# Kernel tuning notes

Measured on AMD Instinct MI355X. Metric: run time of the kernel, lower is better.

The kernel has to match this reference:

```python
import jax, jax.numpy as jnp
import numpy as np

EMB = 16      # importance embedding channels (ch 0 = logit, 1: = cov features)
NSEG = 196    # n_segments (14x14 superpixel grid)
MC = 16       # num_monte_carlo
TEMP = 1.0    # initial Gumbel/RelaxedBernoulli temperature (compute_temperature(0))
JITTER = 1e-3 # numerical_stability_check: diagonal jitter so Cholesky succeeds


def setup_inputs() -> dict:
    key = jax.random.key(0)
    k1, k2, k3 = jax.random.split(key, 3)
    B, C, H, W = 16, 3, 224, 224
    x = jax.random.normal(k1, (B, C, H, W), jnp.float32)
    groups = jax.random.randint(k2, (B, H, W), 0, NSEG, jnp.int32)
    W_conv = jax.random.normal(k3, (EMB, C), jnp.float32) * 0.1
    b_conv = jnp.zeros((EMB,), jnp.float32)
    return {"x": x, "groups": groups, "W_conv": W_conv, "b_conv": b_conv}


def _group_mean(groups, emb):
    # scatter_reduce(mean, include_self=False): per-batch segment mean, 0 for empty groups
    # emb: [B,E,H,W], groups: [B,H,W] -> [B, NSEG, E]
    B, E, H, W = emb.shape
    flat = emb.reshape(B, E, H * W).transpose(0, 2, 1).reshape(B * H * W, E)
    ids = (groups.reshape(B, H * W).astype(jnp.int32)
           + NSEG * jnp.arange(B, dtype=jnp.int32)[:, None]).reshape(-1)
    sums = jax.ops.segment_sum(flat, ids, num_segments=B * NSEG).reshape(B, NSEG, E)
    cnt = jax.ops.segment_sum(jnp.ones((B * H * W,), flat.dtype), ids,
                              num_segments=B * NSEG).reshape(B, NSEG, 1)
    return sums / jnp.maximum(cnt, 1.0)


def reference(x, groups, W_conv, b_conv):
    B, C, H, W = x.shape
    # importance_predictor as 1x1 conv: [B,C,H,W] -> [B,EMB,H,W]
    emb = jnp.einsum('bchw,ec->behw', x, W_conv) + b_conv[None, :, None, None]

    avg = _group_mean(groups, emb)            # [B, NSEG, EMB]
    mu = avg[:, :, 0]                          # [B, NSEG]
    gemb = avg[:, :, 1:]                       # [B, NSEG, EMB-1]
    # groups_emb.mT @ groups_emb (groups_emb is [B, EMB-1, NSEG] in torch)
    sigma = jnp.einsum('bse,bte->bst', gemb, gemb)
    sigma = sigma + JITTER * jnp.eye(NSEG, dtype=sigma.dtype)

    pixel_probs = jax.nn.sigmoid(emb[:, 0])    # [B, H, W]
    group_probs = jax.nn.sigmoid(mu)           # [B, NSEG]

    # MultivariateNormal(mu, sigma).rsample([MC]).movedim(0,-1)
    L = jnp.linalg.cholesky(sigma)             # [B, NSEG, NSEG]
    kg, ku = jax.random.split(jax.random.key(42))
    eps = jax.random.normal(kg, (B, NSEG, MC), x.dtype)
    logits_mc = mu[:, :, None] + jnp.einsum('bst,btm->bsm', L, eps)  # [B,NSEG,MC]

    # RelaxedBernoulli(temp, probs=sigmoid(logits_mc)).rsample()
    u = jax.random.uniform(ku, (B, NSEG, MC), x.dtype, 1e-6, 1.0 - 1e-6)
    logistic = jnp.log(u) - jnp.log1p(-u)
    relaxed = jax.nn.sigmoid((logits_mc + logistic) / TEMP)
    hard = (relaxed > 0.5).astype(relaxed.dtype)
    groups_mcmc = hard + relaxed - jax.lax.stop_gradient(relaxed)  # straight-through

    # groups_to_mask: gather group decision back to every pixel
    gf = groups.reshape(B, H * W).astype(jnp.int32)
    idx = jnp.broadcast_to(gf[:, :, None], (B, H * W, MC))
    mask = jnp.take_along_axis(groups_mcmc, idx, axis=1)           # [B, HW, MC]
    mask = mask.reshape(B, H, W, MC)
    mask = jnp.broadcast_to(mask[:, None], (B, C, H, W, MC))       # expand channels
    return mask, group_probs, pixel_probs, sigma
```

## Files before the change

kernel.cpp:

```cpp
#include <hip/hip_runtime.h>
#include <stdint.h>

#define HW    50176
#define BATCH 16
#define NSEG  196
#define EMB   16
#define MC    16
#define JITTER 0.001f
#define EBLK  14
#define PXB   3584

__host__ __device__ inline void threefry2x32(uint32_t k0, uint32_t k1,
                                             uint32_t x0, uint32_t x1,
                                             uint32_t& o0, uint32_t& o1) {
  uint32_t k2 = k0 ^ k1 ^ 0x1BD11BDAu;
#define TFR(r) { x0 += x1; x1 = (x1 << (r)) | (x1 >> (32 - (r))); x1 ^= x0; }
  x0 += k0; x1 += k1;
  TFR(13) TFR(15) TFR(26) TFR(6)
  x0 += k1; x1 += k2 + 1u;
  TFR(17) TFR(29) TFR(16) TFR(24)
  x0 += k2; x1 += k0 + 2u;
  TFR(13) TFR(15) TFR(26) TFR(6)
  x0 += k0; x1 += k1 + 3u;
  TFR(17) TFR(29) TFR(16) TFR(24)
  x0 += k1; x1 += k2 + 4u;
  TFR(13) TFR(15) TFR(26) TFR(6)
  x0 += k2; x1 += k0 + 5u;
#undef TFR
  o0 = x0; o1 = x1;
}

__device__ inline float erfinv_f32(float x) {
  float w = -log1pf(-x * x);
  float p;
  if (w < 5.0f) {
    w = w - 2.5f;
    p = 2.81022636e-08f;
    p = 3.43273939e-07f + p * w;
    p = -3.5233877e-06f + p * w;
    p = -4.39150654e-06f + p * w;
    p = 0.00021858087f + p * w;
    p = -0.00125372503f + p * w;
    p = -0.00417768164f + p * w;
    p = 0.246640727f + p * w;
    p = 1.50140941f + p * w;
  } else {
    w = sqrtf(w) - 3.0f;
    p = -0.000200214257f;
    p = 0.000100950558f + p * w;
    p = 0.00134934322f + p * w;
    p = -0.00367342844f + p * w;
    p = 0.00573950773f + p * w;
    p = -0.0076224613f + p * w;
    p = 0.00943887047f + p * w;
    p = 1.00167406f + p * w;
    p = 2.83297682f + p * w;
  }
  return p * x;
}

__device__ inline float bits_to_f01(uint32_t bits) {
  uint32_t fb = (bits >> 9) | 0x3F800000u;
  return __uint_as_float(fb) - 1.0f;
}

__device__ inline float dot15(const float a[15], const float b[15]) {
  float d = 0.0f;
#pragma unroll
  for (int j = 0; j < 15; ++j) d = fmaf(a[j], b[j], d);
  return d;
}

__device__ inline void pivot_scalars(const float gk[15], float& invd,
                                     float& dd, float& beta) {
  const float sj = 0.031622776601683794f;
  float t0 = fmaf(gk[0], gk[0], JITTER);
  float t1 = gk[1] * gk[1];   float t2 = gk[2] * gk[2];
  float t3 = gk[3] * gk[3];   float t4 = gk[4] * gk[4];
  float t5 = gk[5] * gk[5];   float t6 = gk[6] * gk[6];
  float t7 = gk[7] * gk[7];   float t8 = gk[8] * gk[8];
  float t9 = gk[9] * gk[9];   float t10 = gk[10] * gk[10];
  float t11 = gk[11] * gk[11]; float t12 = gk[12] * gk[12];
  float t13 = gk[13] * gk[13]; float t14 = gk[14] * gk[14];
  float u0 = t0 + t1, u1 = t2 + t3, u2 = t4 + t5, u3 = t6 + t7;
  float u4 = t8 + t9, u5 = t10 + t11, u6 = t12 + t13;
  float v0 = u0 + u1, v1 = u2 + u3, v2 = u4 + u5, v3 = u6 + t14;
  float jn = (v0 + v1) + (v2 + v3);
  invd = __builtin_amdgcn_rsqf(jn);
  dd = jn * invd;
  beta = (invd * invd) * __builtin_amdgcn_rcpf(fmaf(sj, invd, 1.0f));
}

__global__ __launch_bounds__(256) void emb_kernel(
    const float* __restrict__ x, const int* __restrict__ groups,
    const float* __restrict__ Wc, const float* __restrict__ bc,
    float* __restrict__ partial, float* __restrict__ pixel_probs) {
  __shared__ float lsum[4 * NSEG];
  int b = blockIdx.x / EBLK;
  int blk = blockIdx.x % EBLK;
  int tid = threadIdx.x;
  for (int i = tid; i < 4 * NSEG; i += 256) lsum[i] = 0.0f;
  __syncthreads();
  const float* xb = x + (size_t)b * 3 * HW;
  float w0 = Wc[0], w1 = Wc[1], w2 = Wc[2], b0 = bc[0];
  for (int k = 0; k < PXB / 256; ++k) {
    int p = blk * PXB + k * 256 + tid;
    float x0 = xb[p], x1 = xb[HW + p], x2 = xb[2 * HW + p];
    int g = groups[b * HW + p];
    float e = w0 * x0 + w1 * x1;
    e = e + w2 * x2 + b0;
    pixel_probs[b * HW + p] = 1.0f / (1.0f + expf(-e));
    atomicAdd(&lsum[g], x0);
    atomicAdd(&lsum[NSEG + g], x1);
    atomicAdd(&lsum[2 * NSEG + g], x2);
    atomicAdd(&lsum[3 * NSEG + g], 1.0f);
  }
  __syncthreads();
  float* pb = partial + (size_t)blockIdx.x * (4 * NSEG);
  if (tid < NSEG) {
#pragma unroll
    for (int c = 0; c < 4; ++c) pb[c * NSEG + tid] = lsum[c * NSEG + tid];
  }
}

__global__ __launch_bounds__(256, 1) void main_kernel(
    const float* __restrict__ partial, const float* __restrict__ Wc,
    const float* __restrict__ bc,
    uint32_t kg0, uint32_t kg1, uint32_t ku0, uint32_t ku1,
    float* __restrict__ group_probs, float* __restrict__ sigma_out,
    float* __restrict__ hard) {
  int bid = blockIdx.x;
  int tid = threadIdx.x;

  if (bid < 112) {
    int b = bid / 7;
    int tile = bid % 7;
    __shared__ float ge_s[15][NSEG];
    if (tid < NSEG) {
      float sx0 = 0.0f, sx1 = 0.0f, sx2 = 0.0f, cn = 0.0f;
      for (int bb = 0; bb < EBLK; ++bb) {
        const float* pb = partial + (size_t)(b * EBLK + bb) * (4 * NSEG);
        sx0 += pb[tid]; sx1 += pb[NSEG + tid];
        sx2 += pb[2 * NSEG + tid]; cn += pb[3 * NSEG + tid];
      }
      float denom = fmaxf(cn, 1.0f);
#pragma unroll
      for (int j = 1; j < EMB; ++j) {
        float e = Wc[j * 3 + 0] * sx0 + Wc[j * 3 + 1] * sx1;
        e = e + Wc[j * 3 + 2] * sx2 + bc[j] * cn;
        ge_s[j - 1][tid] = e / denom;
      }
    }
    __syncthreads();
    if (tid < NSEG) {
      int t = tid;
      float gt[15];
#pragma unroll
      for (int j = 0; j < 15; ++j) gt[j] = ge_s[j][t];
      for (int r = 0; r < 28; ++r) {
        int s = tile * 28 + r;
        float a = 0.0f;
#pragma unroll
        for (int j = 0; j < 15; ++j) a = fmaf(ge_s[j][s], gt[j], a);
        if (s == t) a += JITTER;
        sigma_out[((size_t)b * NSEG + s) * NSEG + t] = a;
      }
    }
    return;
  }

  int b = bid - 112;
  __shared__ float ge[15][NSEG];
  __shared__ float mu_l[NSEG];
  __shared__ float eps_lds[NSEG * MC];
  __shared__ __align__(16) float pbuf[2][4][16];

  for (int t = tid; t < NSEG * MC; t += 256) {
    uint32_t a0, a1;
    threefry2x32(kg0, kg1, 0u, (uint32_t)(b * NSEG * MC + t), a0, a1);
    float f = bits_to_f01(a0 ^ a1);
    const float lo = -0.99999994f;
    float u = fmaxf(lo, f * (1.0f - lo) + lo);
    eps_lds[t] = 1.4142135623730951f * erfinv_f32(u);
  }

  if (tid < NSEG) {
    float sx0 = 0.0f, sx1 = 0.0f, sx2 = 0.0f, cn = 0.0f;
    for (int bb = 0; bb < EBLK; ++bb) {
      const float* pb = partial + (size_t)(b * EBLK + bb) * (4 * NSEG);
      sx0 += pb[tid]; sx1 += pb[NSEG + tid];
      sx2 += pb[2 * NSEG + tid]; cn += pb[3 * NSEG + tid];
    }
    float denom = fmaxf(cn, 1.0f);
#pragma unroll
    for (int j = 0; j < EMB; ++j) {
      float e = Wc[j * 3 + 0] * sx0 + Wc[j * 3 + 1] * sx1;
      e = e + Wc[j * 3 + 2] * sx2 + bc[j] * cn;
      float v = e / denom;
      if (j == 0) {
        mu_l[tid] = v;
        group_probs[b * NSEG + tid] = 1.0f / (1.0f + expf(-v));
      } else {
        ge[j - 1][tid] = v;
      }
    }
  }
  __syncthreads();

  int i = tid;
  float g[15];
#pragma unroll
  for (int j = 0; j < 15; ++j) g[j] = (i < NSEG) ? ge[j][i] : 0.0f;
  float acc[16];
#pragma unroll
  for (int m = 0; m < 16; ++m) acc[m] = 0.0f;
  if (tid < 4) {
    float* pw = &pbuf[0][tid][0];
#pragma unroll
    for (int j = 0; j < 15; ++j) pw[j] = g[j];
  }
  __syncthreads();

#define APPLY_PIVOT(rv, invd_, dd_, beta_, K)                               \
  {                                                                         \
    float dot = dot15(g, rv);                                               \
    float w = (i > (K)) ? dot * (invd_)                                     \
                        : ((i == (K)) ? (dd_) : 0.0f);                      \
    const float4* ep = (const float4*)(eps_lds + (K) * MC);                 \
    float4 e0 = ep[0], e1 = ep[1], e2 = ep[2], e3 = ep[3];                  \
    float ek[16] = {e0.x, e0.y, e0.z, e0.w, e1.x, e1.y, e1.z, e1.w,         \
                    e2.x, e2.y, e2.z, e2.w, e3.x, e3.y, e3.z, e3.w};        \
    _Pragma("unroll")                                                       \
    for (int m = 0; m < 16; ++m) acc[m] = fmaf(w, ek[m], acc[m]);           \
    float bd = (beta_) * dot;                                               \
    _Pragma("unroll")                                                       \
    for (int j = 0; j < 15; ++j) g[j] = fmaf(-bd, rv[j], g[j]);             \
  }

  for (int t49 = 0; t49 < 49; ++t49) {
    const float* pb0 = &pbuf[t49 & 1][0][0];
    float r0[15], r1[15], r2[15], r3[15];
    {
      float4 a0 = *(const float4*)(pb0 + 0);
      float4 a1 = *(const float4*)(pb0 + 4);
      float4 a2 = *(const float4*)(pb0 + 8);
      float4 a3 = *(const float4*)(pb0 + 12);
      r0[0]=a0.x; r0[1]=a0.y; r0[2]=a0.z; r0[3]=a0.w;
      r0[4]=a1.x; r0[5]=a1.y; r0[6]=a1.z; r0[7]=a1.w;
      r0[8]=a2.x; r0[9]=a2.y; r0[10]=a2.z; r0[11]=a2.w;
      r0[12]=a3.x; r0[13]=a3.y; r0[14]=a3.z;
      a0 = *(const float4*)(pb0 + 16); a1 = *(const float4*)(pb0 + 20);
      a2 = *(const float4*)(pb0 + 24); a3 = *(const float4*)(pb0 + 28);
      r1[0]=a0.x; r1[1]=a0.y; r1[2]=a0.z; r1[3]=a0.w;
      r1[4]=a1.x; r1[5]=a1.y; r1[6]=a1.z; r1[7]=a1.w;
      r1[8]=a2.x; r1[9]=a2.y; r1[10]=a2.z; r1[11]=a2.w;
      r1[12]=a3.x; r1[13]=a3.y; r1[14]=a3.z;
      a0 = *(const float4*)(pb0 + 32); a1 = *(const float4*)(pb0 + 36);
      a2 = *(const float4*)(pb0 + 40); a3 = *(const float4*)(pb0 + 44);
      r2[0]=a0.x; r2[1]=a0.y; r2[2]=a0.z; r2[3]=a0.w;
      r2[4]=a1.x; r2[5]=a1.y; r2[6]=a1.z; r2[7]=a1.w;
      r2[8]=a2.x; r2[9]=a2.y; r2[10]=a2.z; r2[11]=a2.w;
      r2[12]=a3.x; r2[13]=a3.y; r2[14]=a3.z;
      a0 = *(const float4*)(pb0 + 48); a1 = *(const float4*)(pb0 + 52);
      a2 = *(const float4*)(pb0 + 56); a3 = *(const float4*)(pb0 + 60);
      r3[0]=a0.x; r3[1]=a0.y; r3[2]=a0.z; r3[3]=a0.w;
      r3[4]=a1.x; r3[5]=a1.y; r3[6]=a1.z; r3[7]=a1.w;
      r3[8]=a2.x; r3[9]=a2.y; r3[10]=a2.z; r3[11]=a2.w;
      r3[12]=a3.x; r3[13]=a3.y; r3[14]=a3.z;
    }
    float invd0, dd0, beta0, invd1, dd1, beta1;
    float invd2, dd2, beta2, invd3, dd3, beta3;
    pivot_scalars(r0, invd0, dd0, beta0);
    {
      float d = dot15(r1, r0); float bd = beta0 * d;
#pragma unroll
      for (int j = 0; j < 15; ++j) r1[j] = fmaf(-bd, r0[j], r1[j]);
    }
    pivot_scalars(r1, invd1, dd1, beta1);
    {
      float d = dot15(r2, r0); float bd = beta0 * d;
#pragma unroll
      for (int j = 0; j < 15; ++j) r2[j] = fmaf(-bd, r0[j], r2[j]);
      d = dot15(r2, r1); bd = beta1 * d;
#pragma unroll
      for (int j = 0; j < 15; ++j) r2[j] = fmaf(-bd, r1[j], r2[j]);
    }
    pivot_scalars(r2, invd2, dd2, beta2);
    {
      float d = dot15(r3, r0); float bd = beta0 * d;
#pragma unroll
      for (int j = 0; j < 15; ++j) r3[j] = fmaf(-bd, r0[j], r3[j]);
      d = dot15(r3, r1); bd = beta1 * d;
#pragma unroll
      for (int j = 0; j < 15; ++j) r3[j] = fmaf(-bd, r1[j], r3[j]);
      d = dot15(r3, r2); bd = beta2 * d;
#pragma unroll
      for (int j = 0; j < 15; ++j) r3[j] = fmaf(-bd, r2[j], r3[j]);
    }
    pivot_scalars(r3, invd3, dd3, beta3);

    int k0 = 4 * t49;
    APPLY_PIVOT(r0, invd0, dd0, beta0, k0 + 0)
    APPLY_PIVOT(r1, invd1, dd1, beta1, k0 + 1)
    APPLY_PIVOT(r2, invd2, dd2, beta2, k0 + 2)
    APPLY_PIVOT(r3, invd3, dd3, beta3, k0 + 3)

    int nb = 4 * (t49 + 1);
    if (i >= nb && i < nb + 4) {
      float* pw = &pbuf[(t49 + 1) & 1][i - nb][0];
#pragma unroll
      for (int j = 0; j < 15; ++j) pw[j] = g[j];
    }
    __syncthreads();
  }
#undef APPLY_PIVOT

  if (i < NSEG) {
    float mui = mu_l[i];
    float4 outv[4];
    float* op = (float*)outv;
#pragma unroll
    for (int m = 0; m < 16; ++m) {
      uint32_t a0, a1;
      threefry2x32(ku0, ku1, 0u, (uint32_t)(b * NSEG * MC + i * MC + m), a0, a1);
      float f = bits_to_f01(a0 ^ a1);
      const float mn = 1e-6f;
      const float mx = (float)(1.0 - 1e-6);
      float uu = fmaxf(mn, f * (mx - mn) + mn);
      float lg = logf(uu) - log1pf(-uu);
      float z = mui + acc[m] + lg;
      op[m] = (z > 0.0f) ? 1.0f : 0.0f;
    }
    float4* hp = (float4*)(hard + ((size_t)b * NSEG + i) * MC);
#pragma unroll
    for (int q = 0; q < 4; ++q) hp[q] = outv[q];
  }
}

__global__ __launch_bounds__(256) void mask_kernel(
    const int* __restrict__ groups, const float* __restrict__ hard,
    float4* __restrict__ out) {
  int f = blockIdx.x * blockDim.x + threadIdx.x;
  if (f >= BATCH * 3 * HW * 4) return;
  int pix = f >> 2;
  int q = f & 3;
  int b = pix / (3 * HW);
  int p = pix % HW;
  int g = groups[b * HW + p];
  out[f] = ((const float4*)hard)[(b * NSEG + g) * 4 + q];
}

extern "C" void kernel_launch(void* const* d_in, const int* in_sizes, int n_in,
                              void* d_out, int out_size, void* d_ws, size_t ws_size,
                              hipStream_t stream) {
  const float* x = (const float*)d_in[0];
  const int* groups = (const int*)d_in[1];
  const float* Wc = (const float*)d_in[2];
  const float* bc = (const float*)d_in[3];

  float* out = (float*)d_out;
  float* mask_out = out;
  float* gp_out = out + 38535168;
  float* pp_out = gp_out + 3136;
  float* sig_out = pp_out + 802816;

  float* ws = (float*)d_ws;
  float* partial = ws;
  float* hard    = ws + 175616;

  emb_kernel<<<BATCH * EBLK, 256, 0, stream>>>(x, groups, Wc, bc, partial, pp_out);

  uint32_t kg0, kg1, ku0, ku1;
  threefry2x32(0u, 42u, 0u, 0u, kg0, kg1);
  threefry2x32(0u, 42u, 0u, 1u, ku0, ku1);

  main_kernel<<<128, 256, 0, stream>>>(partial, Wc, bc, kg0, kg1, ku0, ku1,
                                       gp_out, sig_out, hard);
  mask_kernel<<<(BATCH * 3 * HW * 4 + 255) / 256, 256, 0, stream>>>(
      groups, hard, (float4*)mask_out);
}
```

Baseline: 252.2 us.

## Factor next Cholesky panel in owning wave via readlane lookahead

Replaces the per-step redundant 4-row panel factorization done by every thread with a lookahead scheme. The wave that owns the next four pivot rows factors them using readlane broadcasts and publishes the pivot rows and scalars to LDS. All other waves then just apply the published panel. This removes redundant per-thread pivot computation and overlaps panel factorization with the trailing update. In exchange the owning wave does extra serial work and the barrier count is unchanged.

Measured after the change: 262.1 us. 3.9% more time.

```diff
diff --git a/kernel.cpp b/kernel.cpp
--- a/kernel.cpp
+++ b/kernel.cpp
@@ -64,6 +64,10 @@
   return __uint_as_float(fb) - 1.0f;
 }
 
+__device__ inline float readlane_f(float v, int lane) {
+  return __int_as_float(__builtin_amdgcn_readlane(__float_as_int(v), lane));
+}
+
 __device__ inline float dot15(const float a[15], const float b[15]) {
   float d = 0.0f;
 #pragma unroll
@@ -170,10 +174,12 @@
   }
 
   int b = bid - 112;
+  int lane = tid & 63;
+  int wave = tid >> 6;
   __shared__ float ge[15][NSEG];
   __shared__ float mu_l[NSEG];
   __shared__ float eps_lds[NSEG * MC];
-  __shared__ __align__(16) float pbuf[2][4][16];
+  __shared__ __align__(16) float pfin[2][4][20];
 
   for (int t = tid; t < NSEG * MC; t += 256) {
     uint32_t a0, a1;
@@ -214,16 +220,10 @@
   float acc[16];
 #pragma unroll
   for (int m = 0; m < 16; ++m) acc[m] = 0.0f;
-  if (tid < 4) {
-    float* pw = &pbuf[0][tid][0];
-#pragma unroll
-    for (int j = 0; j < 15; ++j) pw[j] = g[j];
-  }
-  __syncthreads();
-
-#define APPLY_PIVOT(rv, invd_, dd_, beta_, K)                               \
+
+#define APPLY_CORE(gkA, invd_, dd_, beta_, K)                               \
   {                                                                         \
-    float dot = dot15(g, rv);                                               \
+    float dot = dot15(g, gkA);                                              \
     float w = (i > (K)) ? dot * (invd_)                                     \
                         : ((i == (K)) ? (dd_) : 0.0f);                      \
     const float4* ep = (const float4*)(eps_lds + (K) * MC);                 \
@@ -234,86 +234,60 @@
     for (int m = 0; m < 16; ++m) acc[m] = fmaf(w, ek[m], acc[m]);           \
     float bd = (beta_) * dot;                                               \
     _Pragma("unroll")                                                       \
-    for (int j = 0; j < 15; ++j) g[j] = fmaf(-bd, rv[j], g[j]);             \
-  }
-
-  for (int t49 = 0; t49 < 49; ++t49) {
-    const float* pb0 = &pbuf[t49 & 1][0][0];
-    float r0[15], r1[15], r2[15], r3[15];
-    {
-      float4 a0 = *(const float4*)(pb0 + 0);
-      float4 a1 = *(const float4*)(pb0 + 4);
-      float4 a2 = *(const float4*)(pb0 + 8);
-      float4 a3 = *(const float4*)(pb0 + 12);
-      r0[0]=a0.x; r0[1]=a0.y; r0[2]=a0.z; r0[3]=a0.w;
-      r0[4]=a1.x; r0[5]=a1.y; r0[6]=a1.z; r0[7]=a1.w;
-      r0[8]=a2.x; r0[9]=a2.y; r0[10]=a2.z; r0[11]=a2.w;
-      r0[12]=a3.x; r0[13]=a3.y; r0[14]=a3.z;
-      a0 = *(const float4*)(pb0 + 16); a1 = *(const float4*)(pb0 + 20);
-      a2 = *(const float4*)(pb0 + 24); a3 = *(const float4*)(pb0 + 28);
-      r1[0]=a0.x; r1[1]=a0.y; r1[2]=a0.z; r1[3]=a0.w;
-      r1[4]=a1.x; r1[5]=a1.y; r1[6]=a1.z; r1[7]=a1.w;
-      r1[8]=a2.x; r1[9]=a2.y; r1[10]=a2.z; r1[11]=a2.w;
-      r1[12]=a3.x; r1[13]=a3.y; r1[14]=a3.z;
-      a0 = *(const float4*)(pb0 + 32); a1 = *(const float4*)(pb0 + 36);
-      a2 = *(const float4*)(pb0 + 40); a3 = *(const float4*)(pb0 + 44);
-      r2[0]=a0.x; r2[1]=a0.y; r2[2]=a0.z; r2[3]=a0.w;
-      r2[4]=a1.x; r2[5]=a1.y; r2[6]=a1.z; r2[7]=a1.w;
-      r2[8]=a2.x; r2[9]=a2.y; r2[10]=a2.z; r2[11]=a2.w;
-      r2[12]=a3.x; r2[13]=a3.y; r2[14]=a3.z;
-      a0 = *(const float4*)(pb0 + 48); a1 = *(const float4*)(pb0 + 52);
-      a2 = *(const float4*)(pb0 + 56); a3 = *(const float4*)(pb0 + 60);
-      r3[0]=a0.x; r3[1]=a0.y; r3[2]=a0.z; r3[3]=a0.w;
-      r3[4]=a1.x; r3[5]=a1.y; r3[6]=a1.z; r3[7]=a1.w;
-      r3[8]=a2.x; r3[9]=a2.y; r3[10]=a2.z; r3[11]=a2.w;
-      r3[12]=a3.x; r3[13]=a3.y; r3[14]=a3.z;
-    }
-    float invd0, dd0, beta0, invd1, dd1, beta1;
-    float invd2, dd2, beta2, invd3, dd3, beta3;
-    pivot_scalars(r0, invd0, dd0, beta0);
-    {
-      float d = dot15(r1, r0); float bd = beta0 * d;
-#pragma unroll
-      for (int j = 0; j < 15; ++j) r1[j] = fmaf(-bd, r0[j], r1[j]);
-    }
-    pivot_scalars(r1, invd1, dd1, beta1);
-    {
-      float d = dot15(r2, r0); float bd = beta0 * d;
-#pragma unroll
-      for (int j = 0; j < 15; ++j) r2[j] = fmaf(-bd, r0[j], r2[j]);
-      d = dot15(r2, r1); bd = beta1 * d;
-#pragma unroll
-      for (int j = 0; j < 15; ++j) r2[j] = fmaf(-bd, r1[j], r2[j]);
-    }
-    pivot_scalars(r2, invd2, dd2, beta2);
-    {
-      float d = dot15(r3, r0); float bd = beta0 * d;
-#pragma unroll
-      for (int j = 0; j < 15; ++j) r3[j] = fmaf(-bd, r0[j], r3[j]);
-      d = dot15(r3, r1); bd = beta1 * d;
-#pragma unroll
-      for (int j = 0; j < 15; ++j) r3[j] = fmaf(-bd, r1[j], r3[j]);
-      d = dot15(r3, r2); bd = beta2 * d;
-#pragma unroll
-      for (int j = 0; j < 15; ++j) r3[j] = fmaf(-bd, r2[j], r3[j]);
-    }
-    pivot_scalars(r3, invd3, dd3, beta3);
-
-    int k0 = 4 * t49;
-    APPLY_PIVOT(r0, invd0, dd0, beta0, k0 + 0)
-    APPLY_PIVOT(r1, invd1, dd1, beta1, k0 + 1)
-    APPLY_PIVOT(r2, invd2, dd2, beta2, k0 + 2)
-    APPLY_PIVOT(r3, invd3, dd3, beta3, k0 + 3)
-
-    int nb = 4 * (t49 + 1);
-    if (i >= nb && i < nb + 4) {
-      float* pw = &pbuf[(t49 + 1) & 1][i - nb][0];
-#pragma unroll
-      for (int j = 0; j < 15; ++j) pw[j] = g[j];
+    for (int j = 0; j < 15; ++j) g[j] = fmaf(-bd, gkA[j], g[j]);            \
+  }
+
+#define FACTOR_PANEL(P)                                                     \
+  for (int kk = 0; kk < 4; ++kk) {                                          \
+    int k = 4 * (P) + kk;                                                   \
+    int ol = k & 63;                                                        \
+    float gk[15];                                                           \
+    _Pragma("unroll")                                                       \
+    for (int j = 0; j < 15; ++j) gk[j] = readlane_f(g[j], ol);              \
+    float invd, dd, beta;                                                   \
+    pivot_scalars(gk, invd, dd, beta);                                      \
+    if (lane == 0) {                                                        \
+      float* pw = &pfin[(P) & 1][kk][0];                                    \
+      _Pragma("unroll")                                                     \
+      for (int j = 0; j < 15; ++j) pw[j] = gk[j];                           \
+      pw[15] = invd; pw[16] = dd; pw[17] = beta;                            \
+    }                                                                       \
+    APPLY_CORE(gk, invd, dd, beta, k)                                       \
+  }
+
+  __syncthreads();
+  int pre = -1;
+  if (wave == 0) {
+    FACTOR_PANEL(0)
+    pre = 0;
+  }
+  __syncthreads();
+
+  for (int q = 0; q < 49; ++q) {
+    if (pre != q) {
+      for (int kk = 0; kk < 4; ++kk) {
+        const float* pv = &pfin[q & 1][kk][0];
+        float4 a0 = *(const float4*)(pv);
+        float4 a1 = *(const float4*)(pv + 4);
+        float4 a2 = *(const float4*)(pv + 8);
+        float4 a3 = *(const float4*)(pv + 12);
+        float gk[15] = {a0.x, a0.y, a0.z, a0.w, a1.x, a1.y, a1.z, a1.w,
+                        a2.x, a2.y, a2.z, a2.w, a3.x, a3.y, a3.z};
+        float invd = a3.w;
+        float dd = pv[16];
+        float beta = pv[17];
+        APPLY_CORE(gk, invd, dd, beta, 4 * q + kk)
+      }
+    }
+    int nq = q + 1;
+    if (nq < 49 && wave == (nq >> 4)) {
+      FACTOR_PANEL(nq)
+      pre = nq;
     }
     __syncthreads();
   }
-#undef APPLY_PIVOT
+#undef FACTOR_PANEL
+#undef APPLY_CORE
 
   if (i < NSEG) {
     float mui = mu_l[i];
```
